# Kernel tuning notes

Measured on AMD Instinct MI355X. Metric: run time of the kernel, lower is better.

Reference implementation:

```python
import jax, jax.numpy as jnp
import numpy as np

TMIN, TMAX, SHIFT = 0, 64, 8
T = (TMAX - TMIN + 1 + 2 * SHIFT) - 1  # period from extended window = 80


def setup_inputs() -> dict:
    key = jax.random.key(0)
    k1, k2, k3, k4 = jax.random.split(key, 4)
    B, S = 8, 4096
    nOut, nIn, nBasis = 8, 8, 17
    a = jax.random.normal(k1, (B, 1, 1, 1, S), dtype=jnp.float32)
    b = jax.random.normal(k2, (B, 1, 1, 1, S), dtype=jnp.float32)
    c = jax.random.normal(k3, (B, 1, 1, 1, S), dtype=jnp.float32)
    coefs = jax.random.normal(k4, (nOut, nIn, nBasis), dtype=jnp.float32)
    return {"a": a, "b": b, "c": c, "coefs": coefs}


def reference(a, b, c, coefs):
    # time embedding (non-extended): (1,1,1,nWin,1)
    t_emb = jnp.arange(TMIN, TMAX + 1, dtype=jnp.float32).reshape(1, 1, 1, -1, 1)
    x = c * (t_emb - b)                      # (B,1,1,nWin,S)
    nBasis = coefs.shape[-1]
    maxN = nBasis // 2
    n = jnp.arange(1, maxN + 1, dtype=jnp.float32)
    norm = 1.0 / jnp.sqrt(jnp.float32(T) / 2)
    ang = (2 * jnp.pi / T) * x[..., None] * n  # (B,1,1,nWin,S,maxN)
    sin_h = jnp.sin(ang) * norm
    cos_h = jnp.cos(ang) * norm
    # interleave sin/cos exactly like torch.stack(...,-1).reshape -> (B,1,1,nWin,S,2*maxN)
    constN = jnp.stack([sin_h, cos_h], axis=-1).reshape(*sin_h.shape[:-1], 2 * maxN)
    cN = constN[:, 0, 0]                     # (B,nWin,S,2*maxN) squeeze singleton chan dims
    const0 = 1.0 / (jnp.sqrt(jnp.float32(2.0)) * jnp.sqrt(jnp.float32(T) / 2))
    dc = const0 * coefs[..., 0]              # (nOut,nIn)
    # out[b,o,i,w,s] = dc[o,i] + sum_n cN[b,w,s,n] * coefs[o,i,1+n]
    out = dc[None, :, :, None, None] + jnp.einsum('bwsn,oin->boiws', cN, coefs[..., 1:])
    return a * out                           # (B,nOut,nIn,nWin,S)
```

## Files before the change

### kernel.cpp

```cpp
#include <hip/hip_runtime.h>
#include <math.h>


constexpr int S_LEN = 4096;
constexpr int W_LEN = 65;
constexpr int NOI   = 64;
constexpr int NB    = 16;
constexpr int NCOEF = 17;

using f4 = __attribute__((ext_vector_type(4))) float;

__global__ __launch_bounds__(256)
void fourier_basis_trf_kernel(const float* __restrict__ a,
                              const float* __restrict__ b,
                              const float* __restrict__ c,
                              const float* __restrict__ coefs,
                              float* __restrict__ out)
{
    const int tid = threadIdx.x;

    const int hw = blockIdx.x;
    const int g  = (hw & 7) * 65 + (hw >> 3);

    const float K    = 6.283185307179586f / 80.0f;
    const float NORM = 0.15811388300841897f;
    const float RS2  = 0.7071067811865476f;

    #pragma unroll 1
    for (int k = 0; k < 4; ++k) {
        const int u      = g * 4 + k;
        const int w      = u % W_LEN;
        const int bs     = u / W_LEN;
        const int schunk = bs & 3;
        const int bb     = bs >> 2;
        const int s0     = (schunk * 256 + tid) * 4;

        const int abi = bb * S_LEN + s0;
        const f4 av = *reinterpret_cast<const f4*>(a + abi);
        const f4 bv = *reinterpret_cast<const f4*>(b + abi);
        const f4 cv = *reinterpret_cast<const f4*>(c + abi);

        const float tf = (float)w;

        const float a0 = av.x * NORM;
        const float a1 = av.y * NORM;
        const float a2 = av.z * NORM;
        const float a3 = av.w * NORM;

        float bas[NB][4];
        {
            const float xv[4] = { cv.x * (tf - bv.x), cv.y * (tf - bv.y),
                                  cv.z * (tf - bv.z), cv.w * (tf - bv.w) };
            #pragma unroll
            for (int j = 0; j < 4; ++j) {
                float sn, cs;
                sincosf(K * xv[j], &sn, &cs);
                bas[0][j] = sn;
                bas[1][j] = cs;
                float sk = sn, ck = cs;
                #pragma unroll
                for (int kk = 1; kk < 8; ++kk) {
                    const float s2 = fmaf(sk, cs,  ck * sn);
                    const float c2 = fmaf(ck, cs, -sk * sn);
                    bas[2 * kk][j]     = s2;
                    bas[2 * kk + 1][j] = c2;
                    sk = s2;
                    ck = c2;
                }
            }
        }

        float* outp = out + ((size_t)bb * NOI * W_LEN + w) * S_LEN + s0;
        constexpr size_t OI_STRIDE = (size_t)W_LEN * S_LEN;

        #pragma unroll 2
        for (int oi = 0; oi < NOI; ++oi) {
            const float* cw = coefs + oi * NCOEF;
            const float d = cw[0] * RS2;
            float x0 = d, x1 = d, x2 = d, x3 = d;
            #pragma unroll
            for (int n = 0; n < NB; ++n) {
                const float cn = cw[1 + n];
                x0 = fmaf(bas[n][0], cn, x0);
                x1 = fmaf(bas[n][1], cn, x1);
                x2 = fmaf(bas[n][2], cn, x2);
                x3 = fmaf(bas[n][3], cn, x3);
            }
            f4 r;
            r.x = x0 * a0;
            r.y = x1 * a1;
            r.z = x2 * a2;
            r.w = x3 * a3;
            *reinterpret_cast<f4*>(outp + (size_t)oi * OI_STRIDE) = r;
        }
    }
}

extern "C" void kernel_launch(void* const* d_in, const int* in_sizes, int n_in,
                              void* d_out, int out_size, void* d_ws, size_t ws_size,
                              hipStream_t stream)
{
    const float* a     = (const float*)d_in[0];
    const float* b     = (const float*)d_in[1];
    const float* c     = (const float*)d_in[2];
    const float* coefs = (const float*)d_in[3];
    float* out = (float*)d_out;

    const dim3 grid(520);
    const dim3 block(256);
    fourier_basis_trf_kernel<<<grid, block, 0, stream>>>(a, b, c, coefs, out);
}
```

Before: 134.9 us.

## Reorganize per (batch,oi) blocks with incremental angle rotation and Chebyshev harmonics

```diff
diff --git a/kernel.cpp b/kernel.cpp
--- a/kernel.cpp
+++ b/kernel.cpp
@@ -4,8 +4,6 @@
 
 constexpr int S_LEN = 4096;
 constexpr int W_LEN = 65;
-constexpr int NOI   = 64;
-constexpr int NB    = 16;
 constexpr int NCOEF = 17;
 
 using f4 = __attribute__((ext_vector_type(4))) float;
@@ -20,79 +18,80 @@
     const int tid = threadIdx.x;
 
     const int hw = blockIdx.x;
-    const int g  = (hw & 7) * 65 + (hw >> 3);
+    const int lg = (hw & 7) * 256 + (hw >> 3);
+    const int bb   = lg >> 8;
+    const int rest = lg & 255;
+    const int oi   = rest >> 2;
+    const int wc   = rest & 3;
+    const int w0   = wc * 16 + (wc ? 1 : 0);
+    const int nw   = wc ? 16 : 17;
 
     const float K    = 6.283185307179586f / 80.0f;
     const float NORM = 0.15811388300841897f;
     const float RS2  = 0.7071067811865476f;
 
-    #pragma unroll 1
-    for (int k = 0; k < 4; ++k) {
-        const int u      = g * 4 + k;
-        const int w      = u % W_LEN;
-        const int bs     = u / W_LEN;
-        const int schunk = bs & 3;
-        const int bb     = bs >> 2;
-        const int s0     = (schunk * 256 + tid) * 4;
+    const float* cw = coefs + oi * NCOEF;
+    const float dterm = cw[0] * RS2;
 
-        const int abi = bb * S_LEN + s0;
+    float sA[16];
+    float sT[16], cT[16];
+    float sD[16], cD[16];
+
+    #pragma unroll
+    for (int j = 0; j < 4; ++j) {
+        const int abi = bb * S_LEN + j * 1024 + tid * 4;
         const f4 av = *reinterpret_cast<const f4*>(a + abi);
         const f4 bv = *reinterpret_cast<const f4*>(b + abi);
         const f4 cv = *reinterpret_cast<const f4*>(c + abi);
+        #pragma unroll
+        for (int k = 0; k < 4; ++k) {
+            const int col = j * 4 + k;
+            const float cc  = cv[k];
+            const float th0 = K * cc * ((float)w0 - bv[k]);
+            const float de  = K * cc;
+            sincosf(th0, &sT[col], &cT[col]);
+            sincosf(de,  &sD[col], &cD[col]);
+            sA[col] = av[k] * NORM;
+        }
+    }
 
-        const float tf = (float)w;
+    float* op = out + ((size_t)(bb * 64 + oi) * W_LEN + w0) * S_LEN + tid * 4;
 
-        const float a0 = av.x * NORM;
-        const float a1 = av.y * NORM;
-        const float a2 = av.z * NORM;
-        const float a3 = av.w * NORM;
+    #pragma unroll 1
+    for (int w = 0; w < nw; ++w) {
+        f4 r[4];
+        #pragma unroll
+        for (int col = 0; col < 16; ++col) {
+            const float s1 = sT[col];
+            const float c1 = cT[col];
+            const float two_c1 = c1 + c1;
 
-        float bas[NB][4];
-        {
-            const float xv[4] = { cv.x * (tf - bv.x), cv.y * (tf - bv.y),
-                                  cv.z * (tf - bv.z), cv.w * (tf - bv.w) };
+            float acc = dterm;
+            acc = fmaf(s1, cw[1], acc);
+            acc = fmaf(c1, cw[2], acc);
+            float s2 = two_c1 * s1;
+            float c2 = fmaf(two_c1, c1, -1.0f);
+            acc = fmaf(s2, cw[3], acc);
+            acc = fmaf(c2, cw[4], acc);
+            float spp = s1, sp = s2, cpp = c1, cp = c2;
             #pragma unroll
-            for (int j = 0; j < 4; ++j) {
-                float sn, cs;
-                sincosf(K * xv[j], &sn, &cs);
-                bas[0][j] = sn;
-                bas[1][j] = cs;
-                float sk = sn, ck = cs;
-                #pragma unroll
-                for (int kk = 1; kk < 8; ++kk) {
-                    const float s2 = fmaf(sk, cs,  ck * sn);
-                    const float c2 = fmaf(ck, cs, -sk * sn);
-                    bas[2 * kk][j]     = s2;
-                    bas[2 * kk + 1][j] = c2;
-                    sk = s2;
-                    ck = c2;
-                }
+            for (int n = 3; n <= 8; ++n) {
+                const float sn = fmaf(two_c1, sp, -spp);
+                const float cn = fmaf(two_c1, cp, -cpp);
+                acc = fmaf(sn, cw[2 * n - 1], acc);
+                acc = fmaf(cn, cw[2 * n],     acc);
+                spp = sp; sp = sn;
+                cpp = cp; cp = cn;
             }
+            r[col >> 2][col & 3] = acc * sA[col];
+
+            sT[col] = fmaf(s1, cD[col],  c1 * sD[col]);
+            cT[col] = fmaf(c1, cD[col], -(s1 * sD[col]));
         }
-
-        float* outp = out + ((size_t)bb * NOI * W_LEN + w) * S_LEN + s0;
-        constexpr size_t OI_STRIDE = (size_t)W_LEN * S_LEN;
-
-        #pragma unroll 2
-        for (int oi = 0; oi < NOI; ++oi) {
-            const float* cw = coefs + oi * NCOEF;
-            const float d = cw[0] * RS2;
-            float x0 = d, x1 = d, x2 = d, x3 = d;
-            #pragma unroll
-            for (int n = 0; n < NB; ++n) {
-                const float cn = cw[1 + n];
-                x0 = fmaf(bas[n][0], cn, x0);
-                x1 = fmaf(bas[n][1], cn, x1);
-                x2 = fmaf(bas[n][2], cn, x2);
-                x3 = fmaf(bas[n][3], cn, x3);
-            }
-            f4 r;
-            r.x = x0 * a0;
-            r.y = x1 * a1;
-            r.z = x2 * a2;
-            r.w = x3 * a3;
-            *reinterpret_cast<f4*>(outp + (size_t)oi * OI_STRIDE) = r;
-        }
+        #pragma unroll
+        for (int j = 0; j < 4; ++j)
+            *reinterpret_cast<f4*>(op + j * 1024) = r[j];
+        op += S_LEN;
     }
 }
 
@@ -106,7 +105,7 @@
     const float* coefs = (const float*)d_in[3];
     float* out = (float*)d_out;
 
-    const dim3 grid(520);
+    const dim3 grid(2048);
     const dim3 block(256);
     fourier_basis_trf_kernel<<<grid, block, 0, stream>>>(a, b, c, coefs, out);
 }
```

After: 136.9 us. Within noise of the previous version (+1.5%).
